# Kernel tuning notes

Measured on AMD Instinct MI355X. Metric: run time of the kernel, lower is better.

The kernel has to match this reference:

```python
import jax, jax.numpy as jnp
import numpy as np

NB_HEAD = 8
SIZE_PER_HEAD = 64
MAX_LEN = 1024
MASK_PENALTY = 1e12


def setup_inputs() -> dict:
    key = jax.random.key(0)
    ks = jax.random.split(key, 6)
    B, L, D_IN = 8, MAX_LEN, 512
    D_OUT = NB_HEAD * SIZE_PER_HEAD
    return {
        "Q_seq": jax.random.normal(ks[0], (B, L, D_IN), dtype=jnp.float32),
        "K_seq": jax.random.normal(ks[1], (B, L, D_IN), dtype=jnp.float32),
        "V_seq": jax.random.normal(ks[2], (B, L, D_IN), dtype=jnp.float32),
        "WQ": jax.random.normal(ks[3], (D_IN, D_OUT), dtype=jnp.float32) * 0.03,
        "WK": jax.random.normal(ks[4], (D_IN, D_OUT), dtype=jnp.float32) * 0.03,
        "WV": jax.random.normal(ks[5], (D_IN, D_OUT), dtype=jnp.float32) * 0.03,
    }


def reference(Q_seq, K_seq, V_seq, WQ, WK, WV):
    B, L, _ = Q_seq.shape
    H, D = NB_HEAD, SIZE_PER_HEAD
    # project and split heads: [B, L, H*D] -> [B, H, L, D]
    q = (Q_seq @ WQ).reshape(B, L, H, D).transpose(0, 2, 1, 3)
    k = (K_seq @ WK).reshape(B, L, H, D).transpose(0, 2, 1, 3)
    v = (V_seq @ WV).reshape(B, L, H, D).transpose(0, 2, 1, 3)
    scale = 1.0 / jnp.sqrt(jnp.asarray(D, dtype=q.dtype))
    scores = jnp.einsum('bhqd,bhkd->bhqk', q, k) * scale  # [B,H,L,L]
    # Mask(): eye+cumsum construction == causal mask (penalize key > query)
    causal = jnp.triu(jnp.ones((L, L), dtype=scores.dtype), k=1)
    scores = scores - causal * MASK_PENALTY
    A = jax.nn.softmax(scores, axis=-1)
    O = jnp.einsum('bhqk,bhkd->bhqd', A, v)  # [B,H,L,D]
    return O.transpose(0, 2, 1, 3).reshape(B, L, H * D)
```

## Files before the change

kernel.cpp:

```cpp
#include <hip/hip_runtime.h>

#define NH 8
#define DH 64
#define SL 1024
#define NB 8
#define DIN 512
#define DOUT 512
#define PS 72

typedef __bf16 bf16x8 __attribute__((ext_vector_type(8)));
typedef float floatx4 __attribute__((ext_vector_type(4)));
typedef unsigned short ushortx8 __attribute__((ext_vector_type(8)));

__device__ __forceinline__ unsigned short f2bf(float f) {
    unsigned int u = __builtin_bit_cast(unsigned int, f);
    u += 0x7FFFu + ((u >> 16) & 1u);
    return (unsigned short)(u >> 16);
}

__device__ __forceinline__ floatx4 mfma_bf16(bf16x8 a, bf16x8 b, floatx4 c) {
    return __builtin_amdgcn_mfma_f32_16x16x32_bf16(a, b, c, 0, 0, 0);
}

__device__ __forceinline__ void gld_lds16(const unsigned short* g, unsigned short* l) {
    __builtin_amdgcn_global_load_lds(
        (const __attribute__((address_space(1))) unsigned int*)g,
        (__attribute__((address_space(3))) unsigned int*)l, 16, 0, 0);
}

__device__ __forceinline__ unsigned int pack_bf2(float a, float b) {
    return __builtin_amdgcn_perm(__builtin_bit_cast(unsigned int, b),
                                 __builtin_bit_cast(unsigned int, a), 0x07060302u);
}

__global__ __launch_bounds__(256) void prep_kernel(const float* __restrict__ Qs,
                                                   const float* __restrict__ Ks,
                                                   const float* __restrict__ Vs,
                                                   const float* __restrict__ WQ,
                                                   const float* __restrict__ WK,
                                                   const float* __restrict__ WV,
                                                   unsigned short* __restrict__ xb,
                                                   unsigned short* __restrict__ wt) {
    __shared__ unsigned short tile[64][68];
    const int bid = blockIdx.x;
    if (bid < 6144) {
        const int z = bid >> 11;
        const float* X = (z == 0) ? Qs : (z == 1 ? Ks : Vs);
        const int t = (bid & 2047) * 256 + threadIdx.x;
        const int row = t >> 6, c = t & 63;
        const float4 a = *(const float4*)(X + t * 8);
        const float4 b = *(const float4*)(X + t * 8 + 4);
        ushortx8 o;
        o[0] = f2bf(a.x); o[1] = f2bf(a.y); o[2] = f2bf(a.z); o[3] = f2bf(a.w);
        o[4] = f2bf(b.x); o[5] = f2bf(b.y); o[6] = f2bf(b.z); o[7] = f2bf(b.w);
        const int dst = (((row >> 7) * 8 + (c >> 3)) * 128 + (row & 127)) * 64 +
                        (((c & 7) ^ (row & 7)) * 8);
        *(ushortx8*)(xb + z * 8192 * DIN + dst) = o;
    } else {
        const int b2 = bid - 6144;
        const int z = b2 >> 6;
        const int r = b2 & 63;
        const float* W = (z == 0) ? WQ : (z == 1 ? WK : WV);
        const int k0 = (r >> 3) * 64, n0 = (r & 7) * 64;
        const int tn = threadIdx.x & 63, tk = threadIdx.x >> 6;
#pragma unroll
        for (int i = 0; i < 16; ++i) {
            const int kk = tk + i * 4;
            tile[tn][kk] = f2bf(W[(k0 + kk) * DOUT + n0 + tn]);
        }
        __syncthreads();
#pragma unroll
        for (int i = 0; i < 16; ++i) {
            const int nn = tk + i * 4;
            const int n = n0 + nn, k = k0 + tn;
            const int dst = (((z * 4 + (n >> 7)) * 8 + (k >> 6)) * 128 + (n & 127)) * 64 +
                            ((((k >> 3) & 7) ^ (n & 7)) * 8) + (k & 7);
            wt[dst] = tile[nn][tn];
        }
    }
}

__global__ __launch_bounds__(256) void proj_kernel(const unsigned short* __restrict__ xbt,
                                                   const unsigned short* __restrict__ wtt,
                                                   unsigned short* __restrict__ qw,
                                                   unsigned short* __restrict__ ks,
                                                   unsigned short* __restrict__ vs) {
    __shared__ __align__(16) unsigned short S[32768];
    const int z = blockIdx.y;
    const int wg = blockIdx.x;
    const int ix = wg >> 3;
    const int mblk = (wg & 7) * 8 + (ix >> 2);
    const int nblk = ix & 3;
    const int w = threadIdx.x >> 6, lane = threadIdx.x & 63;
    const int l15 = lane & 15, quad = lane >> 4;
    const int wm = w >> 1, wn = w & 1;
    const int soff = lane * 8;
    const unsigned short* Ab = xbt + z * (8192 * DIN) + mblk * 8 * 8192 + (w * 4) * 512 + soff;
    const unsigned short* Bb = wtt + (z * 4 + nblk) * 8 * 8192 + (w * 4) * 512 + soff;

    floatx4 acc[4][4];
#pragma unroll
    for (int i = 0; i < 4; ++i)
#pragma unroll
        for (int j = 0; j < 4; ++j) acc[i][j] = floatx4{0.f, 0.f, 0.f, 0.f};

    auto STAGE = [&](int buf, int kblk) {
        unsigned short* Asw = &S[buf * 16384 + (w * 4) * 512];
        unsigned short* Bsw = &S[buf * 16384 + 8192 + (w * 4) * 512];
#pragma unroll
        for (int i = 0; i < 4; ++i) {
            gld_lds16(Ab + kblk * 8192 + i * 512, Asw + i * 512);
            gld_lds16(Bb + kblk * 8192 + i * 512, Bsw + i * 512);
        }
    };

    auto COMPUTE = [&](int buf) {
        const unsigned short* Asb = &S[buf * 16384];
        const unsigned short* Bsb = &S[buf * 16384 + 8192];
#pragma unroll
        for (int ksub = 0; ksub < 2; ++ksub) {
            bf16x8 af[4], bfr[4];
#pragma unroll
            for (int mi = 0; mi < 4; ++mi) {
                const int row = wm * 64 + mi * 16 + l15;
                af[mi] = *(const bf16x8*)&Asb[row * 64 + (((quad + ksub * 4) ^ (l15 & 7)) * 8)];
            }
#pragma unroll
            for (int nt = 0; nt < 4; ++nt) {
                const int row = wn * 64 + nt * 16 + l15;
                bfr[nt] = *(const bf16x8*)&Bsb[row * 64 + (((quad + ksub * 4) ^ (l15 & 7)) * 8)];
            }
#pragma unroll
            for (int mi = 0; mi < 4; ++mi)
#pragma unroll
                for (int nt = 0; nt < 4; ++nt)
                    acc[mi][nt] = mfma_bf16(af[mi], bfr[nt], acc[mi][nt]);
        }
    };

    STAGE(0, 0);
    __syncthreads();
    for (int kblk = 0; kblk < 7; ++kblk) {
        STAGE((kblk + 1) & 1, kblk + 1);
        COMPUTE(kblk & 1);
        __syncthreads();
    }
    COMPUTE(1);

    __syncthreads();
#pragma unroll
    for (int mi = 0; mi < 4; ++mi)
#pragma unroll
        for (int nt = 0; nt < 4; ++nt)
#pragma unroll
            for (int r = 0; r < 4; ++r) {
                const int a = wm * 64 + mi * 16 + quad * 4 + r;
                const int c = wn * 64 + nt * 16 + l15;
                const int h = c >> 6, dh = c & 63;
                float v = acc[mi][nt][r];
                int lidx;
                if (z == 0) {
                    v *= 0.18033688f;
                    lidx = h * 8192 + (a >> 4) * 1024 + (dh >> 3) * 128 + (a & 15) * 8 + (dh & 7);
                } else if (z == 1) {
                    lidx = (((((h << 3) + (a >> 4)) << 1) | (dh >> 5))) * 512 +
                           (a & 15) * 32 + (dh & 31);
                } else {
                    const int s64 = ((a & 15) << 2) | ((a >> 4) & 3);
                    lidx = ((((h << 1) | (a >> 6)) << 1) | (s64 >> 5)) * 2048 +
                           dh * 32 + (s64 & 31);
                }
                S[lidx] = f2bf(v);
            }
    __syncthreads();

    const int b = mblk >> 3;
    const int li0 = (mblk & 7) * 128;
    const int tid = threadIdx.x;
    unsigned short* outp = (z == 0) ? qw : (z == 1 ? ks : vs);
#pragma unroll
    for (int j = 0; j < 8; ++j) {
        const int off = j * 2048 + tid * 8;
        const ushortx8 val = *(const ushortx8*)(S + off);
        int gidx;
        if (z == 0) {
            const int h = off >> 13, o13 = off & 8191;
            gidx = ((b * 8 + nblk * 2 + h) * 64 + (li0 >> 4) + (o13 >> 10)) * 1024 + (o13 & 1023);
        } else if (z == 1) {
            const int region = off >> 9, pos = off & 511;
            const int h = region >> 4, g = (region >> 1) & 7, d5 = region & 1;
            gidx = (((b * 8 + nblk * 2 + h) * 64 + (li0 >> 4) + g) * 2 + d5) * 512 + pos;
        } else {
            const int region = off >> 11, pos = off & 2047;
            const int h = region >> 2, l6 = (region >> 1) & 1, s5 = region & 1;
            gidx = ((b * 8 + nblk * 2 + h) * 32 + (li0 >> 5) + l6 * 2 + s5) * 2048 + pos;
        }
        *(ushortx8*)(outp + gidx) = val;
    }
}

template <bool DOMASK>
__device__ __forceinline__ void frame_step(
    int kt, int m0, int l15, int quad,
    const unsigned short* __restrict__ ksb,
    const unsigned short* __restrict__ vsb,
    unsigned short* myPs,
    bf16x8 aQA0, bf16x8 aQA1, bf16x8 aQB0, bf16x8 aQB1,
    floatx4& oA0, floatx4& oA1, floatx4& oA2, floatx4& oA3,
    floatx4& oB0, floatx4& oB1, floatx4& oB2, floatx4& oB3,
    float& lA0, float& lA1, float& lA2, float& lA3,
    float& lB0, float& lB1, float& lB2, float& lB3) {
    const floatx4 zf = {0.f, 0.f, 0.f, 0.f};
    const unsigned short* kp = ksb + (kt >> 4) * 1024;
    floatx4 sA0 = zf, sA1 = zf, sA2 = zf, sA3 = zf;
    floatx4 sB0 = zf, sB1 = zf, sB2 = zf, sB3 = zf;
    __builtin_amdgcn_s_setprio(1);
#define QK_T(T, SA, SB)                                                     \
    if (!DOMASK || (kt + T * 16 <= m0 + 31)) {                              \
        const bf16x8 k0_ = *(const bf16x8*)(kp + T * 1024);                 \
        const bf16x8 k1_ = *(const bf16x8*)(kp + T * 1024 + 512);           \
        if (!DOMASK || (kt + T * 16 <= m0 + 15))                            \
            SA = mfma_bf16(aQA1, k1_, mfma_bf16(aQA0, k0_, zf));            \
        SB = mfma_bf16(aQB1, k1_, mfma_bf16(aQB0, k0_, zf));                \
    }
    QK_T(0, sA0, sB0)
    QK_T(1, sA1, sB1)
    QK_T(2, sA2, sB2)
    QK_T(3, sA3, sB3)
#undef QK_T
    __builtin_amdgcn_s_setprio(0);
    const unsigned short* vb = vsb + (kt >> 5) * 2048;
    const bf16x8 v00 = *(const bf16x8*)(vb);
    const bf16x8 v01 = *(const bf16x8*)(vb + 512);
    const bf16x8 v02 = *(const bf16x8*)(vb + 1024);
    const bf16x8 v03 = *(const bf16x8*)(vb + 1536);
    const bf16x8 v10 = *(const bf16x8*)(vb + 2048);
    const bf16x8 v11 = *(const bf16x8*)(vb + 2560);
    const bf16x8 v12 = *(const bf16x8*)(vb + 3072);
    const bf16x8 v13 = *(const bf16x8*)(vb + 3584);
#define TAIL_R(R, LA, LB)                                                    \
    {                                                                        \
        const int rowA = m0 + quad * 4 + R;                                  \
        float pa0 = __builtin_amdgcn_exp2f(sA0[R]);                          \
        float pa1 = __builtin_amdgcn_exp2f(sA1[R]);                          \
        float pa2 = __builtin_amdgcn_exp2f(sA2[R]);                          \
        float pa3 = __builtin_amdgcn_exp2f(sA3[R]);                          \
        float pb0 = __builtin_amdgcn_exp2f(sB0[R]);                          \
        float pb1 = __builtin_amdgcn_exp2f(sB1[R]);                          \
        float pb2 = __builtin_amdgcn_exp2f(sB2[R]);                          \
        float pb3 = __builtin_amdgcn_exp2f(sB3[R]);                          \
        if (DOMASK) {                                                        \
            if (kt + l15 > rowA) pa0 = 0.f;                                  \
            if (kt + 16 + l15 > rowA) pa1 = 0.f;                             \
            if (kt + 32 + l15 > rowA) pa2 = 0.f;                             \
            if (kt + 48 + l15 > rowA) pa3 = 0.f;                             \
            if (kt + l15 > rowA + 16) pb0 = 0.f;                             \
            if (kt + 16 + l15 > rowA + 16) pb1 = 0.f;                        \
            if (kt + 32 + l15 > rowA + 16) pb2 = 0.f;                        \
            if (kt + 48 + l15 > rowA + 16) pb3 = 0.f;                        \
        }                                                                    \
        LA += (pa0 + pa1) + (pa2 + pa3);                                     \
        LB += (pb0 + pb1) + (pb2 + pb3);                                     \
        uint2 pkA, pkB;                                                      \
        pkA.x = pack_bf2(pa0, pa1);                                          \
        pkA.y = pack_bf2(pa2, pa3);                                          \
        pkB.x = pack_bf2(pb0, pb1);                                          \
        pkB.y = pack_bf2(pb2, pb3);                                          \
        *(uint2*)(myPs + (quad * 4 + R) * PS + l15 * 4) = pkA;               \
        *(uint2*)(myPs + (16 + quad * 4 + R) * PS + l15 * 4) = pkB;          \
    }
    TAIL_R(0, lA0, lB0)
    TAIL_R(1, lA1, lB1)
    TAIL_R(2, lA2, lB2)
    TAIL_R(3, lA3, lB3)
#undef TAIL_R
    __builtin_amdgcn_wave_barrier();
    const bf16x8 aPA0 = *(const bf16x8*)(myPs + l15 * PS + quad * 8);
    const bf16x8 aPA1 = *(const bf16x8*)(myPs + l15 * PS + 32 + quad * 8);
    const bf16x8 aPB0 = *(const bf16x8*)(myPs + (16 + l15) * PS + quad * 8);
    const bf16x8 aPB1 = *(const bf16x8*)(myPs + (16 + l15) * PS + 32 + quad * 8);
    __builtin_amdgcn_wave_barrier();
    __builtin_amdgcn_s_setprio(1);
    oA0 = mfma_bf16(aPA1, v10, mfma_bf16(aPA0, v00, oA0));
    oA1 = mfma_bf16(aPA1, v11, mfma_bf16(aPA0, v01, oA1));
    oA2 = mfma_bf16(aPA1, v12, mfma_bf16(aPA0, v02, oA2));
    oA3 = mfma_bf16(aPA1, v13, mfma_bf16(aPA0, v03, oA3));
    oB0 = mfma_bf16(aPB1, v10, mfma_bf16(aPB0, v00, oB0));
    oB1 = mfma_bf16(aPB1, v11, mfma_bf16(aPB0, v01, oB1));
    oB2 = mfma_bf16(aPB1, v12, mfma_bf16(aPB0, v02, oB2));
    oB3 = mfma_bf16(aPB1, v13, mfma_bf16(aPB0, v03, oB3));
    __builtin_amdgcn_s_setprio(0);
}

__global__ __launch_bounds__(256) void attn_kernel(const unsigned short* __restrict__ qw,
                                                   const unsigned short* __restrict__ ksp,
                                                   const unsigned short* __restrict__ vsp,
                                                   float* __restrict__ out) {
    __shared__ union {
        unsigned short Ps[4][32 * PS];
        float Cb[2][64][42];
    } sh;
    const int w = threadIdx.x >> 6;
    const int lane = threadIdx.x & 63;
    const int l15 = lane & 15, quad = lane >> 4;
    const int s_ = blockIdx.x;
    const int xcd = s_ & 7;
    const int idx = s_ >> 3;
    const int bh = xcd * 8 + (idx & 7);
    const int xb16 = idx >> 3;
    const int b = bh >> 3, h = bh & 7;
    const int p = (w < 2) ? xb16 : 31 - xb16;
    const int half = w & 1;
    const int m0 = p * 32;

    const unsigned short* qpA = qw + (bh * 64 + 2 * p) * 1024 + quad * 128 + l15 * 8;
    const bf16x8 aQA0 = *(const bf16x8*)qpA;
    const bf16x8 aQA1 = *(const bf16x8*)(qpA + 512);
    const bf16x8 aQB0 = *(const bf16x8*)(qpA + 1024);
    const bf16x8 aQB1 = *(const bf16x8*)(qpA + 1536);

    const unsigned short* ksb = ksp + (bh * 64) * 2 * 512 + l15 * 32 + quad * 8;
    const unsigned short* vsb = vsp + (bh * 32 * 64 + l15) * 32 + quad * 8;
    unsigned short* myPs = sh.Ps[w];

    const floatx4 zf = {0.f, 0.f, 0.f, 0.f};
    floatx4 oA0 = zf, oA1 = zf, oA2 = zf, oA3 = zf;
    floatx4 oB0 = zf, oB1 = zf, oB2 = zf, oB3 = zf;
    float lA0 = 0.f, lA1 = 0.f, lA2 = 0.f, lA3 = 0.f;
    float lB0 = 0.f, lB1 = 0.f, lB2 = 0.f, lB3 = 0.f;

    const int nf = (m0 + 95) >> 6;
    const int last = nf - 1;
    for (int j = half; j < last; j += 2)
        frame_step<false>(j * 64, m0, l15, quad, ksb, vsb, myPs,
                          aQA0, aQA1, aQB0, aQB1,
                          oA0, oA1, oA2, oA3, oB0, oB1, oB2, oB3,
                          lA0, lA1, lA2, lA3, lB0, lB1, lB2, lB3);
    if ((last & 1) == half)
        frame_step<true>(last * 64, m0, l15, quad, ksb, vsb, myPs,
                         aQA0, aQA1, aQB0, aQB1,
                         oA0, oA1, oA2, oA3, oB0, oB1, oB2, oB3,
                         lA0, lA1, lA2, lA3, lB0, lB1, lB2, lB3);

    __syncthreads();
    if (half == 1) {
        float* cb = &sh.Cb[w >> 1][lane][0];
        cb[0] = oA0[0];  cb[1] = oA0[1];  cb[2] = oA0[2];  cb[3] = oA0[3];
        cb[4] = oA1[0];  cb[5] = oA1[1];  cb[6] = oA1[2];  cb[7] = oA1[3];
        cb[8] = oA2[0];  cb[9] = oA2[1];  cb[10] = oA2[2]; cb[11] = oA2[3];
        cb[12] = oA3[0]; cb[13] = oA3[1]; cb[14] = oA3[2]; cb[15] = oA3[3];
        cb[16] = oB0[0]; cb[17] = oB0[1]; cb[18] = oB0[2]; cb[19] = oB0[3];
        cb[20] = oB1[0]; cb[21] = oB1[1]; cb[22] = oB1[2]; cb[23] = oB1[3];
        cb[24] = oB2[0]; cb[25] = oB2[1]; cb[26] = oB2[2]; cb[27] = oB2[3];
        cb[28] = oB3[0]; cb[29] = oB3[1]; cb[30] = oB3[2]; cb[31] = oB3[3];
        cb[32] = lA0; cb[33] = lA1; cb[34] = lA2; cb[35] = lA3;
        cb[36] = lB0; cb[37] = lB1; cb[38] = lB2; cb[39] = lB3;
    }
    __syncthreads();
    if (half == 0) {
        const float* cb = &sh.Cb[w >> 1][lane][0];
        oA0[0] += cb[0];  oA0[1] += cb[1];  oA0[2] += cb[2];  oA0[3] += cb[3];
        oA1[0] += cb[4];  oA1[1] += cb[5];  oA1[2] += cb[6];  oA1[3] += cb[7];
        oA2[0] += cb[8];  oA2[1] += cb[9];  oA2[2] += cb[10]; oA2[3] += cb[11];
        oA3[0] += cb[12]; oA3[1] += cb[13]; oA3[2] += cb[14]; oA3[3] += cb[15];
        oB0[0] += cb[16]; oB0[1] += cb[17]; oB0[2] += cb[18]; oB0[3] += cb[19];
        oB1[0] += cb[20]; oB1[1] += cb[21]; oB1[2] += cb[22]; oB1[3] += cb[23];
        oB2[0] += cb[24]; oB2[1] += cb[25]; oB2[2] += cb[26]; oB2[3] += cb[27];
        oB3[0] += cb[28]; oB3[1] += cb[29]; oB3[2] += cb[30]; oB3[3] += cb[31];
        lA0 += cb[32]; lA1 += cb[33]; lA2 += cb[34]; lA3 += cb[35];
        lB0 += cb[36]; lB1 += cb[37]; lB2 += cb[38]; lB3 += cb[39];
#define OUT_R(R, LA, LB)                                                      \
    {                                                                         \
        float lAr = LA, lBr = LB;                                             \
        lAr += __shfl_xor(lAr, 1); lBr += __shfl_xor(lBr, 1);                 \
        lAr += __shfl_xor(lAr, 2); lBr += __shfl_xor(lBr, 2);                 \
        lAr += __shfl_xor(lAr, 4); lBr += __shfl_xor(lBr, 4);                 \
        lAr += __shfl_xor(lAr, 8); lBr += __shfl_xor(lBr, 8);                 \
        const float invA = 1.0f / lAr;                                        \
        const float invB = 1.0f / lBr;                                        \
        const int rowA = m0 + quad * 4 + R;                                   \
        float* opA = out + (b * SL + rowA) * DOUT + h * DH + l15;             \
        float* opB = opA + 16 * DOUT;                                         \
        opA[0] = oA0[R] * invA;  opA[16] = oA1[R] * invA;                     \
        opA[32] = oA2[R] * invA; opA[48] = oA3[R] * invA;                     \
        opB[0] = oB0[R] * invB;  opB[16] = oB1[R] * invB;                     \
        opB[32] = oB2[R] * invB; opB[48] = oB3[R] * invB;                     \
    }
        OUT_R(0, lA0, lB0)
        OUT_R(1, lA1, lB1)
        OUT_R(2, lA2, lB2)
        OUT_R(3, lA3, lB3)
#undef OUT_R
    }
}

extern "C" void kernel_launch(void* const* d_in, const int* in_sizes, int n_in,
                              void* d_out, int out_size, void* d_ws, size_t ws_size,
                              hipStream_t stream) {
    const float* Qs = (const float*)d_in[0];
    const float* Ks = (const float*)d_in[1];
    const float* Vs = (const float*)d_in[2];
    const float* WQ = (const float*)d_in[3];
    const float* WK = (const float*)d_in[4];
    const float* WV = (const float*)d_in[5];
    float* out = (float*)d_out;

    unsigned short* xb = (unsigned short*)d_ws;
    unsigned short* wt = xb + 3 * 8192 * DIN;
    unsigned short* qw = wt + 3 * DIN * DOUT;
    unsigned short* ks = qw + NB * NH * SL * DH;
    unsigned short* vs = ks + NB * NH * SL * DH;

    prep_kernel<<<dim3(6336), 256, 0, stream>>>(Qs, Ks, Vs, WQ, WK, WV, xb, wt);
    proj_kernel<<<dim3(256, 3), 256, 0, stream>>>(xb, wt, qw, ks, vs);
    attn_kernel<<<dim3(1024), 256, 0, stream>>>(qw, ks, vs, out);
}
```

Baseline: 156.1 us.

## Fuse fp32-to-bf16 activation conversion into projection GEMM load path

The separate prep pass that converts Q/K/V activations to swizzled bf16 in global memory is removed. The projection kernel now loads fp32 rows directly into registers, converts them with packed bf16 conversion instructions, and writes them swizzled into LDS, with the register loads issued before compute to overlap. Only the weight transpose stays as a small kernel. This cuts a full write and re-read of the bf16 activation copy, but the A operand now goes through registers instead of direct global-to-LDS loads, and each projection block reads fp32 (twice the bytes) repeatedly across its 4 N-blocks.

```diff
diff --git a/kernel.cpp b/kernel.cpp
--- a/kernel.cpp
+++ b/kernel.cpp
@@ -33,87 +33,99 @@
                                  __builtin_bit_cast(unsigned int, a), 0x07060302u);
 }
 
-__global__ __launch_bounds__(256) void prep_kernel(const float* __restrict__ Qs,
+__device__ __forceinline__ unsigned int cvt_pk_bf16(float lo, float hi) {
+    unsigned int r;
+    asm("v_cvt_pk_bf16_f32 %0, %1, %2" : "=v"(r) : "v"(lo), "v"(hi));
+    return r;
+}
+
+__global__ __launch_bounds__(256) void wt_kernel(const float* __restrict__ WQ,
+                                                 const float* __restrict__ WK,
+                                                 const float* __restrict__ WV,
+                                                 unsigned short* __restrict__ wt) {
+    __shared__ unsigned short tile[64][68];
+    const int bid = blockIdx.x;
+    const int z = bid >> 6;
+    const int r = bid & 63;
+    const float* W = (z == 0) ? WQ : (z == 1 ? WK : WV);
+    const int k0 = (r >> 3) * 64, n0 = (r & 7) * 64;
+    const int tn = threadIdx.x & 63, tk = threadIdx.x >> 6;
+#pragma unroll
+    for (int i = 0; i < 16; ++i) {
+        const int kk = tk + i * 4;
+        tile[tn][kk] = f2bf(W[(k0 + kk) * DOUT + n0 + tn]);
+    }
+    __syncthreads();
+#pragma unroll
+    for (int i = 0; i < 16; ++i) {
+        const int nn = tk + i * 4;
+        const int n = n0 + nn, k = k0 + tn;
+        const int dst = (((z * 4 + (n >> 7)) * 8 + (k >> 6)) * 128 + (n & 127)) * 64 +
+                        ((((k >> 3) & 7) ^ (n & 7)) * 8) + (k & 7);
+        wt[dst] = tile[nn][tn];
+    }
+}
+
+__global__ __launch_bounds__(256) void proj_kernel(const float* __restrict__ Qs,
                                                    const float* __restrict__ Ks,
                                                    const float* __restrict__ Vs,
-                                                   const float* __restrict__ WQ,
-                                                   const float* __restrict__ WK,
-                                                   const float* __restrict__ WV,
-                                                   unsigned short* __restrict__ xb,
-                                                   unsigned short* __restrict__ wt) {
-    __shared__ unsigned short tile[64][68];
-    const int bid = blockIdx.x;
-    if (bid < 6144) {
-        const int z = bid >> 11;
-        const float* X = (z == 0) ? Qs : (z == 1 ? Ks : Vs);
-        const int t = (bid & 2047) * 256 + threadIdx.x;
-        const int row = t >> 6, c = t & 63;
-        const float4 a = *(const float4*)(X + t * 8);
-        const float4 b = *(const float4*)(X + t * 8 + 4);
-        ushortx8 o;
-        o[0] = f2bf(a.x); o[1] = f2bf(a.y); o[2] = f2bf(a.z); o[3] = f2bf(a.w);
-        o[4] = f2bf(b.x); o[5] = f2bf(b.y); o[6] = f2bf(b.z); o[7] = f2bf(b.w);
-        const int dst = (((row >> 7) * 8 + (c >> 3)) * 128 + (row & 127)) * 64 +
-                        (((c & 7) ^ (row & 7)) * 8);
-        *(ushortx8*)(xb + z * 8192 * DIN + dst) = o;
-    } else {
-        const int b2 = bid - 6144;
-        const int z = b2 >> 6;
-        const int r = b2 & 63;
-        const float* W = (z == 0) ? WQ : (z == 1 ? WK : WV);
-        const int k0 = (r >> 3) * 64, n0 = (r & 7) * 64;
-        const int tn = threadIdx.x & 63, tk = threadIdx.x >> 6;
-#pragma unroll
-        for (int i = 0; i < 16; ++i) {
-            const int kk = tk + i * 4;
-            tile[tn][kk] = f2bf(W[(k0 + kk) * DOUT + n0 + tn]);
-        }
-        __syncthreads();
-#pragma unroll
-        for (int i = 0; i < 16; ++i) {
-            const int nn = tk + i * 4;
-            const int n = n0 + nn, k = k0 + tn;
-            const int dst = (((z * 4 + (n >> 7)) * 8 + (k >> 6)) * 128 + (n & 127)) * 64 +
-                            ((((k >> 3) & 7) ^ (n & 7)) * 8) + (k & 7);
-            wt[dst] = tile[nn][tn];
-        }
-    }
-}
-
-__global__ __launch_bounds__(256) void proj_kernel(const unsigned short* __restrict__ xbt,
                                                    const unsigned short* __restrict__ wtt,
                                                    unsigned short* __restrict__ qw,
                                                    unsigned short* __restrict__ ks,
                                                    unsigned short* __restrict__ vs) {
     __shared__ __align__(16) unsigned short S[32768];
     const int z = blockIdx.y;
+    const float* X = (z == 0) ? Qs : (z == 1 ? Ks : Vs);
     const int wg = blockIdx.x;
     const int ix = wg >> 3;
     const int mblk = (wg & 7) * 8 + (ix >> 2);
     const int nblk = ix & 3;
     const int w = threadIdx.x >> 6, lane = threadIdx.x & 63;
+    const int tid = threadIdx.x;
     const int l15 = lane & 15, quad = lane >> 4;
     const int wm = w >> 1, wn = w & 1;
     const int soff = lane * 8;
-    const unsigned short* Ab = xbt + z * (8192 * DIN) + mblk * 8 * 8192 + (w * 4) * 512 + soff;
     const unsigned short* Bb = wtt + (z * 4 + nblk) * 8 * 8192 + (w * 4) * 512 + soff;
 
+    const int arow = tid >> 1;
+    const int kc0 = (tid & 1) * 4;
+    const float* Xp = X + (size_t)(mblk * 128 + arow) * 512 + (tid & 1) * 32;
+
     floatx4 acc[4][4];
 #pragma unroll
     for (int i = 0; i < 4; ++i)
 #pragma unroll
         for (int j = 0; j < 4; ++j) acc[i][j] = floatx4{0.f, 0.f, 0.f, 0.f};
 
-    auto STAGE = [&](int buf, int kblk) {
-        unsigned short* Asw = &S[buf * 16384 + (w * 4) * 512];
+    float4 aA0, aA1, aA2, aA3, aA4, aA5, aA6, aA7;
+    auto ALOAD = [&](int kblk) {
+        const float* p = Xp + kblk * 64;
+        aA0 = *(const float4*)(p);      aA1 = *(const float4*)(p + 4);
+        aA2 = *(const float4*)(p + 8);  aA3 = *(const float4*)(p + 12);
+        aA4 = *(const float4*)(p + 16); aA5 = *(const float4*)(p + 20);
+        aA6 = *(const float4*)(p + 24); aA7 = *(const float4*)(p + 28);
+    };
+    auto AWRITE = [&](int buf) {
+        unsigned short* base = &S[buf * 16384 + arow * 64];
+        const int rx = arow & 7;
+#define AW(I, LO, HI)                                                      \
+    {                                                                      \
+        uint4 wv;                                                          \
+        wv.x = cvt_pk_bf16(LO.x, LO.y);                                    \
+        wv.y = cvt_pk_bf16(LO.z, LO.w);                                    \
+        wv.z = cvt_pk_bf16(HI.x, HI.y);                                    \
+        wv.w = cvt_pk_bf16(HI.z, HI.w);                                    \
+        *(uint4*)(base + (((kc0 + I) ^ rx) * 8)) = wv;                     \
+    }
+        AW(0, aA0, aA1) AW(1, aA2, aA3) AW(2, aA4, aA5) AW(3, aA6, aA7)
+#undef AW
+    };
+    auto BSTAGE = [&](int buf, int kblk) {
         unsigned short* Bsw = &S[buf * 16384 + 8192 + (w * 4) * 512];
 #pragma unroll
-        for (int i = 0; i < 4; ++i) {
-            gld_lds16(Ab + kblk * 8192 + i * 512, Asw + i * 512);
+        for (int i = 0; i < 4; ++i)
             gld_lds16(Bb + kblk * 8192 + i * 512, Bsw + i * 512);
-        }
     };
-
     auto COMPUTE = [&](int buf) {
         const unsigned short* Asb = &S[buf * 16384];
         const unsigned short* Bsb = &S[buf * 16384 + 8192];
@@ -138,11 +150,15 @@
         }
     };
 
-    STAGE(0, 0);
+    ALOAD(0);
+    BSTAGE(0, 0);
+    AWRITE(0);
     __syncthreads();
     for (int kblk = 0; kblk < 7; ++kblk) {
-        STAGE((kblk + 1) & 1, kblk + 1);
+        ALOAD(kblk + 1);
+        BSTAGE((kblk + 1) & 1, kblk + 1);
         COMPUTE(kblk & 1);
+        AWRITE((kblk + 1) & 1);
         __syncthreads();
     }
     COMPUTE(1);
@@ -176,7 +192,6 @@
 
     const int b = mblk >> 3;
     const int li0 = (mblk & 7) * 128;
-    const int tid = threadIdx.x;
     unsigned short* outp = (z == 0) ? qw : (z == 1 ? ks : vs);
 #pragma unroll
     for (int j = 0; j < 8; ++j) {
@@ -405,13 +420,12 @@
     const float* WV = (const float*)d_in[5];
     float* out = (float*)d_out;
 
-    unsigned short* xb = (unsigned short*)d_ws;
-    unsigned short* wt = xb + 3 * 8192 * DIN;
+    unsigned short* wt = (unsigned short*)d_ws;
     unsigned short* qw = wt + 3 * DIN * DOUT;
     unsigned short* ks = qw + NB * NH * SL * DH;
     unsigned short* vs = ks + NB * NH * SL * DH;
 
-    prep_kernel<<<dim3(6336), 256, 0, stream>>>(Qs, Ks, Vs, WQ, WK, WV, xb, wt);
-    proj_kernel<<<dim3(256, 3), 256, 0, stream>>>(xb, wt, qw, ks, vs);
+    wt_kernel<<<dim3(192), 256, 0, stream>>>(WQ, WK, WV, wt);
+    proj_kernel<<<dim3(256, 3), 256, 0, stream>>>(Qs, Ks, Vs, wt, qw, ks, vs);
     attn_kernel<<<dim3(1024), 256, 0, stream>>>(qw, ks, vs, out);
 }
```

New measurement: 169.7 us. 1.09x slower.
